# Performance work log

Hardware: AMD Instinct MI355X
Metric: run time of the kernel (lower is better)

## Reference

```python
import jax, jax.numpy as jnp
import numpy as np

D_MODEL, N_HEADS, D_K, D_V = 1024, 16, 64, 64
B, S = 4, 2048
EPS = 1e-5


def setup_inputs() -> dict:
    key = jax.random.key(0)
    ks = jax.random.split(key, 8)
    scale = 1.0 / np.sqrt(D_MODEL)
    return {
        "input_Q": jax.random.normal(ks[0], (B, S, D_MODEL), dtype=jnp.float32),
        "input_K": jax.random.normal(ks[1], (B, S, D_MODEL), dtype=jnp.float32),
        "input_V": jax.random.normal(ks[2], (B, S, D_MODEL), dtype=jnp.float32),
        "attn_mask": jax.random.bernoulli(ks[3], 0.15, (B, S, S)),  # True = masked
        "W_Q": jax.random.uniform(ks[4], (N_HEADS * D_K, D_MODEL), jnp.float32, -scale, scale),
        "W_K": jax.random.uniform(ks[5], (N_HEADS * D_K, D_MODEL), jnp.float32, -scale, scale),
        "W_V": jax.random.uniform(ks[6], (N_HEADS * D_V, D_MODEL), jnp.float32, -scale, scale),
        "W_fc": jax.random.uniform(ks[7], (D_MODEL, N_HEADS * D_V), jnp.float32, -scale, scale),
    }


def _proj(x, W, h, d):
    # x: [B,S,D] @ W.T ([D, h*d]) -> [B,h,S,d]
    b, s, _ = x.shape
    y = jnp.einsum("bsd,ed->bse", x, W)
    return y.reshape(b, s, h, d).transpose(0, 2, 1, 3)


def reference(input_Q, input_K, input_V, attn_mask, W_Q, W_K, W_V, W_fc):
    b, s, d_model = input_Q.shape
    Q = _proj(input_Q, W_Q, N_HEADS, D_K)  # [B,H,S,dk]
    K = _proj(input_K, W_K, N_HEADS, D_K)
    V = _proj(input_V, W_V, N_HEADS, D_V)

    scores = jnp.einsum("bhqd,bhkd->bhqk", Q, K) / np.sqrt(D_K).astype(np.float32)
    scores = jnp.where(attn_mask[:, None, :, :], jnp.float32(-1e9), scores)
    attn = jax.nn.softmax(scores, axis=-1)  # [B,H,S,S]

    context = jnp.einsum("bhqk,bhkd->bhqd", attn, V)
    context = context.transpose(0, 2, 1, 3).reshape(b, s, N_HEADS * D_V)
    output = jnp.einsum("bse,de->bsd", context, W_fc)

    x = output + input_Q  # residual
    mu = jnp.mean(x, axis=-1, keepdims=True)
    var = jnp.mean(jnp.square(x - mu), axis=-1, keepdims=True)
    ln = (x - mu) / jnp.sqrt(var + EPS)  # fresh LayerNorm: gamma=1, beta=0
    return ln, attn
```

## Files before the change

### kernel.cpp

```cpp
#include <hip/hip_runtime.h>
#include <cstdint>
#include <cstddef>

constexpr int Bc  = 4;
constexpr int Sc  = 2048;
constexpr int DMc = 1024;
constexpr int Hc  = 16;
constexpr int DHc = 64;
constexpr int BHc = Bc * Hc;

typedef float f32x4  __attribute__((ext_vector_type(4)));
typedef short bf16x8 __attribute__((ext_vector_type(8)));

static __device__ __forceinline__ short f2bf(float x) {
  uint32_t u = __builtin_bit_cast(uint32_t, x);
  u += 0x7fffu + ((u >> 16) & 1u);
  return (short)(u >> 16);
}

static __device__ __forceinline__ f32x4 mfma16(bf16x8 a, bf16x8 b, f32x4 c) {
  return __builtin_amdgcn_mfma_f32_16x16x32_bf16(a, b, c, 0, 0, 0);
}

static __device__ __forceinline__ void gload16(const short* g, short* l) {
  __builtin_amdgcn_global_load_lds(
      (const __attribute__((address_space(1))) void*)g,
      (__attribute__((address_space(3))) void*)l, 16, 0, 0);
}

__global__ __launch_bounds__(256) void k_cvt(const float* __restrict__ in,
                                             short* __restrict__ out) {
  int i = blockIdx.x * 256 + threadIdx.x;
  float4 v = reinterpret_cast<const float4*>(in)[i];
  short4 o;
  o.x = f2bf(v.x); o.y = f2bf(v.y); o.z = f2bf(v.z); o.w = f2bf(v.w);
  reinterpret_cast<short4*>(out)[i] = o;
}

__global__ __launch_bounds__(256) void k_pack(const int* __restrict__ m,
                                              uint32_t* __restrict__ bits) {
  size_t i = (size_t)blockIdx.x * 256 + threadIdx.x;
  uint64_t b = __ballot(m[i] != 0);
  int lane = threadIdx.x & 63;
  if (lane == 0)  bits[i >> 5] = (uint32_t)b;
  if (lane == 32) bits[i >> 5] = (uint32_t)(b >> 32);
}

__global__ __launch_bounds__(256) void k_gemm(const short* __restrict__ A,
                                              const short* __restrict__ Bt,
                                              void* __restrict__ out, int mode) {
  __shared__ __align__(16) short lA[128 * 32];
  __shared__ __align__(16) short lB[128 * 32];
  const int bm = blockIdx.x * 128, bn = blockIdx.y * 128;
  const int lane = threadIdx.x & 63, w = threadIdx.x >> 6;
  const int wr = w >> 1, wc = w & 1;
  const int r = lane & 15, g = lane >> 4;
  const int lrow = lane >> 2;
  const int lsl  = (lane & 3) ^ ((lane >> 3) & 3);
  const int rsw  = (r >> 1) & 3;

  f32x4 acc[4][4] = {};
  const short* Ab = A + (size_t)bm * DMc;
  const short* Bb = Bt + (size_t)bn * DMc;

  for (int k0 = 0; k0 < DMc; k0 += 32) {
    __syncthreads();
    #pragma unroll
    for (int c = 0; c < 2; c++) {
      const int rbase = c * 64 + w * 16;
      gload16(Ab + (size_t)(rbase + lrow) * DMc + k0 + lsl * 8, lA + rbase * 32);
      gload16(Bb + (size_t)(rbase + lrow) * DMc + k0 + lsl * 8, lB + rbase * 32);
    }
    __syncthreads();

    bf16x8 af[4], bfr[4];
    #pragma unroll
    for (int i = 0; i < 4; i++) {
      const int arow = wr * 64 + i * 16 + r;
      af[i]  = *reinterpret_cast<const bf16x8*>(lA + arow * 32 + (g ^ rsw) * 8);
      const int brow = wc * 64 + i * 16 + r;
      bfr[i] = *reinterpret_cast<const bf16x8*>(lB + brow * 32 + (g ^ rsw) * 8);
    }
    #pragma unroll
    for (int i = 0; i < 4; i++)
      #pragma unroll
      for (int n = 0; n < 4; n++) acc[i][n] = mfma16(af[i], bfr[n], acc[i][n]);
  }

  #pragma unroll
  for (int i = 0; i < 4; i++) {
    #pragma unroll
    for (int n = 0; n < 4; n++) {
      const int col = bn + wc * 64 + n * 16 + r;
      #pragma unroll
      for (int j = 0; j < 4; j++) {
        const int m = bm + wr * 64 + i * 16 + g * 4 + j;
        if (mode == 2) {
          reinterpret_cast<float*>(out)[(size_t)m * DMc + col] = acc[i][n][j];
        } else {
          const int b = m >> 11, s = m & (Sc - 1);
          const int h = col >> 6, d = col & (DHc - 1);
          size_t idx = (mode == 1)
              ? ((size_t)(b * Hc + h) * DHc + d) * Sc + s
              : ((size_t)(b * Hc + h) * Sc + s) * DHc + d;
          reinterpret_cast<short*>(out)[idx] = f2bf(acc[i][n][j]);
        }
      }
    }
  }
}

__global__ __launch_bounds__(512, 4) void k_flash(const short* __restrict__ Qb,
                                                  const short* __restrict__ Kb,
                                                  const short* __restrict__ Vt,
                                                  const uint32_t* __restrict__ pbits,
                                                  short* __restrict__ ctx,
                                                  float* __restrict__ rsum) {
  __shared__ __align__(16) short kbuf[2][4096];
  __shared__ __align__(16) short vbuf[2][4096];
  __shared__ __align__(16) short pbuf[8][1024];

  const int qbase = blockIdx.x * 128;
  const int bh = blockIdx.y;
  const int b = bh >> 4, h = bh & 15;
  const int tid = threadIdx.x;
  const int lane = tid & 63, w = tid >> 6;
  const int r = lane & 15, g = lane >> 4;
  const int rx = r & 7;

  const int srow = tid >> 3;
  const int sslot = (tid & 7) ^ (srow & 7);
  const short* ksrc = Kb + ((size_t)bh * Sc + srow) * DHc + sslot * 8;
  const short* vsrc = Vt + ((size_t)bh * DHc + srow) * Sc + sslot * 8;
  short* const kdst0 = &kbuf[0][w * 512];
  short* const kdst1 = &kbuf[1][w * 512];
  short* const vdst0 = &vbuf[0][w * 512];
  short* const vdst1 = &vbuf[1][w * 512];

  const short* qrow = Qb + ((size_t)bh * Sc + qbase + w * 16 + r) * DHc;
  const bf16x8 qf0 = *reinterpret_cast<const bf16x8*>(qrow + g * 8);
  const bf16x8 qf1 = *reinterpret_cast<const bf16x8*>(qrow + g * 8 + 32);

  const uint32_t* mrow = pbits + ((size_t)b * Sc + qbase + w * 16 + r) * (Sc / 32);

  constexpr float SCL = 0.18033688f;
  f32x4 pacc[4] = {};
  float rs = 0.f;

  gload16(ksrc, kdst0);
  gload16(vsrc, vdst0);
  __syncthreads();

  int cur = 0;
  for (int kt = 0; kt < 32; kt++) {
    if (kt + 1 < 32) {
      gload16(ksrc + (size_t)(kt + 1) * 64 * DHc, cur ? kdst0 : kdst1);
      gload16(vsrc + (kt + 1) * 64,               cur ? vdst0 : vdst1);
    }
    const short* kb = kbuf[cur];
    const short* vb = vbuf[cur];

    f32x4 sc4[4];
    #pragma unroll
    for (int tt = 0; tt < 4; tt++) {
      const int krow = (tt * 16 + r) * 64;
      bf16x8 kf0 = *reinterpret_cast<const bf16x8*>(kb + krow + ((g ^ rx) << 3));
      bf16x8 kf1 = *reinterpret_cast<const bf16x8*>(kb + krow + (((g + 4) ^ rx) << 3));
      f32x4 a = {};
      a = mfma16(kf0, qf0, a);
      a = mfma16(kf1, qf1, a);
      sc4[tt] = a;
    }

    const uint2 mu = *reinterpret_cast<const uint2*>(mrow + kt * 2);
    #pragma unroll
    for (int tt = 0; tt < 4; tt++) {
      const uint32_t mword = (tt < 2) ? mu.x : mu.y;
      const int bsh = (tt & 1) * 16 + g * 4;
      f32x4 e;
      #pragma unroll
      for (int j = 0; j < 4; j++) {
        float v = __builtin_exp2f(sc4[tt][j] * SCL);
        if ((mword >> (bsh + j)) & 1u) v = 0.f;
        e[j] = v;
        rs += v;
      }
      uint32_t lo = (uint32_t)(uint16_t)f2bf(e[0]) | ((uint32_t)(uint16_t)f2bf(e[1]) << 16);
      uint32_t hi = (uint32_t)(uint16_t)f2bf(e[2]) | ((uint32_t)(uint16_t)f2bf(e[3]) << 16);
      uint64_t pk = (uint64_t)lo | ((uint64_t)hi << 32);
      *reinterpret_cast<uint64_t*>(
          &pbuf[w][r * 64 + (((tt * 2 + (g >> 1)) ^ rx) << 3) + ((g & 1) << 2)]) = pk;
    }

    #pragma unroll
    for (int kt2 = 0; kt2 < 2; kt2++) {
      const int sl = ((kt2 * 4 + g) ^ rx) << 3;
      const bf16x8 paf = *reinterpret_cast<const bf16x8*>(&pbuf[w][r * 64 + sl]);
      #pragma unroll
      for (int n = 0; n < 4; n++) {
        const bf16x8 vf = *reinterpret_cast<const bf16x8*>(vb + (n * 16 + r) * 64 + sl);
        pacc[n] = mfma16(paf, vf, pacc[n]);
      }
    }

    __syncthreads();
    cur ^= 1;
  }

  rs += __shfl_xor(rs, 16);
  rs += __shfl_xor(rs, 32);

  float riv[4];
  #pragma unroll
  for (int j = 0; j < 4; j++) riv[j] = 1.0f / __shfl(rs, g * 4 + j);

  short* cbase = ctx + ((size_t)b * Sc + qbase + w * 16) * DMc + h * DHc;
  #pragma unroll
  for (int n = 0; n < 4; n++)
    #pragma unroll
    for (int j = 0; j < 4; j++)
      cbase[(size_t)(g * 4 + j) * DMc + n * 16 + r] = f2bf(pacc[n][j] * riv[j]);

  if (lane < 16) rsum[(size_t)bh * Sc + qbase + w * 16 + r] = rs;
}

__global__ __launch_bounds__(512) void k_attnw(const short* __restrict__ Qb,
                                               const short* __restrict__ Kb,
                                               const uint32_t* __restrict__ pbits,
                                               const float* __restrict__ rsum,
                                               float* __restrict__ attn) {
  const int qb = blockIdx.x * 16;
  const int bh = blockIdx.y;
  const int b = bh >> 4;
  const int lane = threadIdx.x & 63, w = threadIdx.x >> 6;
  const int r = lane & 15, g = lane >> 4;

  const short* qrow = Qb + ((size_t)bh * Sc + qb + r) * DHc;
  const bf16x8 qf0 = *reinterpret_cast<const bf16x8*>(qrow + g * 8);
  const bf16x8 qf1 = *reinterpret_cast<const bf16x8*>(qrow + g * 8 + 32);

  const float rinv = 1.0f / rsum[(size_t)bh * Sc + qb + r];

  const uint32_t* mrow = pbits + ((size_t)b * Sc + qb + r) * (Sc / 32) + w * 8;
  const uint4 m0 = *reinterpret_cast<const uint4*>(mrow);
  const uint4 m1 = *reinterpret_cast<const uint4*>(mrow + 4);
  const uint32_t mw[8] = {m0.x, m0.y, m0.z, m0.w, m1.x, m1.y, m1.z, m1.w};

  const short* kbase = Kb + ((size_t)bh * Sc + w * 256) * DHc;
  float* out = attn + ((size_t)bh * Sc + qb + r) * Sc + w * 256;

  constexpr float SCL = 0.18033688f;
  #pragma unroll
  for (int t = 0; t < 16; t++) {
    const short* krow = kbase + (size_t)(t * 16 + r) * DHc;
    bf16x8 kf0 = *reinterpret_cast<const bf16x8*>(krow + g * 8);
    bf16x8 kf1 = *reinterpret_cast<const bf16x8*>(krow + g * 8 + 32);
    f32x4 a = {};
    a = mfma16(kf0, qf0, a);
    a = mfma16(kf1, qf1, a);
    const uint32_t mword = mw[t >> 1];
    const int bsh = (t & 1) * 16 + g * 4;
    f32x4 o;
    #pragma unroll
    for (int j = 0; j < 4; j++) {
      float v = __builtin_exp2f(a[j] * SCL) * rinv;
      if ((mword >> (bsh + j)) & 1u) v = 0.f;
      o[j] = v;
    }
    __builtin_nontemporal_store(o, reinterpret_cast<f32x4*>(out + t * 16 + g * 4));
  }
}

__global__ __launch_bounds__(256) void k_ln(const float* __restrict__ y,
                                            const float* __restrict__ resid,
                                            float* __restrict__ out) {
  const int m = blockIdx.x, t = threadIdx.x;
  const float4 a = reinterpret_cast<const float4*>(y + (size_t)m * DMc)[t];
  const float4 b = reinterpret_cast<const float4*>(resid + (size_t)m * DMc)[t];
  float x0 = a.x + b.x, x1 = a.y + b.y, x2 = a.z + b.z, x3 = a.w + b.w;

  float s = x0 + x1 + x2 + x3;
  #pragma unroll
  for (int m2 = 1; m2 < 64; m2 <<= 1) s += __shfl_xor(s, m2);
  __shared__ float red[4];
  __shared__ float red2[4];
  const int w = t >> 6, lane = t & 63;
  if (lane == 0) red[w] = s;
  __syncthreads();
  const float mean = (red[0] + red[1] + red[2] + red[3]) * (1.0f / DMc);

  x0 -= mean; x1 -= mean; x2 -= mean; x3 -= mean;
  float s2 = x0 * x0 + x1 * x1 + x2 * x2 + x3 * x3;
  #pragma unroll
  for (int m2 = 1; m2 < 64; m2 <<= 1) s2 += __shfl_xor(s2, m2);
  if (lane == 0) red2[w] = s2;
  __syncthreads();
  const float var = (red2[0] + red2[1] + red2[2] + red2[3]) * (1.0f / DMc);
  const float rstd = rsqrtf(var + 1e-5f);

  float4 o;
  o.x = x0 * rstd; o.y = x1 * rstd; o.z = x2 * rstd; o.w = x3 * rstd;
  reinterpret_cast<float4*>(out + (size_t)m * DMc)[t] = o;
}

extern "C" void kernel_launch(void* const* d_in, const int* in_sizes, int n_in,
                              void* d_out, int out_size, void* d_ws, size_t ws_size,
                              hipStream_t stream) {
  const float* inQ = (const float*)d_in[0];
  const float* inK = (const float*)d_in[1];
  const float* inV = (const float*)d_in[2];
  const int*   msk = (const int*)d_in[3];
  const float* WQ  = (const float*)d_in[4];
  const float* WK  = (const float*)d_in[5];
  const float* WV  = (const float*)d_in[6];
  const float* Wfc = (const float*)d_in[7];

  float* out_ln   = (float*)d_out;
  float* out_attn = out_ln + (size_t)Bc * Sc * DMc;

  const size_t NX = (size_t)Bc * Sc * DMc;
  const size_t NW = (size_t)DMc * DMc;
  short* ws = (short*)d_ws;
  short* XbQ = ws;
  short* XbK = XbQ + NX;
  short* XbV = XbK + NX;
  short* WQb = XbV + NX;
  short* WKb = WQb + NW;
  short* WVb = WKb + NW;
  short* Wfb = WVb + NW;
  short* Qb  = Wfb + NW;
  short* Kb  = Qb + NX;
  short* Vt  = Kb + NX;
  uint32_t* pbits = (uint32_t*)(Vt + NX);
  float* rsum = (float*)(pbits + (size_t)Bc * Sc * (Sc / 32));
  short* ctx = XbV;
  float* y   = (float*)XbQ;

  k_cvt<<<dim3((unsigned)(NX / 1024)), 256, 0, stream>>>(inQ, XbQ);
  k_cvt<<<dim3((unsigned)(NX / 1024)), 256, 0, stream>>>(inK, XbK);
  k_cvt<<<dim3((unsigned)(NX / 1024)), 256, 0, stream>>>(inV, XbV);
  k_cvt<<<dim3((unsigned)(NW / 1024)), 256, 0, stream>>>(WQ, WQb);
  k_cvt<<<dim3((unsigned)(NW / 1024)), 256, 0, stream>>>(WK, WKb);
  k_cvt<<<dim3((unsigned)(NW / 1024)), 256, 0, stream>>>(WV, WVb);
  k_cvt<<<dim3((unsigned)(NW / 1024)), 256, 0, stream>>>(Wfc, Wfb);
  k_pack<<<dim3((unsigned)(Bc * Sc * (Sc / 256))), 256, 0, stream>>>(msk, pbits);

  dim3 gp(Bc * Sc / 128, DMc / 128);
  k_gemm<<<gp, 256, 0, stream>>>(XbQ, WQb, (void*)Qb, 0);
  k_gemm<<<gp, 256, 0, stream>>>(XbK, WKb, (void*)Kb, 0);
  k_gemm<<<gp, 256, 0, stream>>>(XbV, WVb, (void*)Vt, 1);

  k_flash<<<dim3(Sc / 128, BHc), 512, 0, stream>>>(Qb, Kb, Vt, pbits, ctx, rsum);

  k_attnw<<<dim3(Sc / 16, BHc), 512, 0, stream>>>(Qb, Kb, pbits, rsum, out_attn);

  k_gemm<<<gp, 256, 0, stream>>>(ctx, Wfb, (void*)y, 2);

  k_ln<<<dim3(Bc * Sc), 256, 0, stream>>>(y, inQ, out_ln);
}
```

Before: 654.0 us.

## Fuse attention-weight output into flash kernel and batch conversion/QKV GEMM launches

Moves the second pass that writes the normalized attention matrix into the end of the flash kernel, using the row sum already held in registers, so the separate attnw kernel and the rsum buffer go away. The seven conversion launches are merged into two kernels, and the three QKV projection GEMMs into one launch using a z grid dimension with templated modes. This cuts launch overhead and the rsum round trip. The cost is a flash kernel whose tail is now dominated by streaming 1 GB of attention writes from only 128-row blocks, which may lower the parallelism available for that write phase.

After: 597.2 us. 1.1x faster.

```diff
diff --git a/kernel.cpp b/kernel.cpp
--- a/kernel.cpp
+++ b/kernel.cpp
@@ -28,8 +28,32 @@
       (__attribute__((address_space(3))) void*)l, 16, 0, 0);
 }
 
-__global__ __launch_bounds__(256) void k_cvt(const float* __restrict__ in,
-                                             short* __restrict__ out) {
+__global__ __launch_bounds__(256) void k_cvt3(const float* __restrict__ a,
+                                              const float* __restrict__ b,
+                                              const float* __restrict__ c,
+                                              short* __restrict__ oa,
+                                              short* __restrict__ ob,
+                                              short* __restrict__ oc) {
+  const float* in = blockIdx.y == 0 ? a : (blockIdx.y == 1 ? b : c);
+  short* out      = blockIdx.y == 0 ? oa : (blockIdx.y == 1 ? ob : oc);
+  int i = blockIdx.x * 256 + threadIdx.x;
+  float4 v = reinterpret_cast<const float4*>(in)[i];
+  short4 o;
+  o.x = f2bf(v.x); o.y = f2bf(v.y); o.z = f2bf(v.z); o.w = f2bf(v.w);
+  reinterpret_cast<short4*>(out)[i] = o;
+}
+
+__global__ __launch_bounds__(256) void k_cvtw(const float* __restrict__ a,
+                                              const float* __restrict__ b,
+                                              const float* __restrict__ c,
+                                              const float* __restrict__ d,
+                                              short* __restrict__ oa,
+                                              short* __restrict__ ob,
+                                              short* __restrict__ oc,
+                                              short* __restrict__ od) {
+  const int y = blockIdx.y;
+  const float* in = y == 0 ? a : (y == 1 ? b : (y == 2 ? c : d));
+  short* out      = y == 0 ? oa : (y == 1 ? ob : (y == 2 ? oc : od));
   int i = blockIdx.x * 256 + threadIdx.x;
   float4 v = reinterpret_cast<const float4*>(in)[i];
   short4 o;
@@ -46,12 +70,13 @@
   if (lane == 32) bits[i >> 5] = (uint32_t)(b >> 32);
 }
 
-__global__ __launch_bounds__(256) void k_gemm(const short* __restrict__ A,
-                                              const short* __restrict__ Bt,
-                                              void* __restrict__ out, int mode) {
+template <int MODE>
+static __device__ __forceinline__ void gemm_body(const short* __restrict__ A,
+                                                 const short* __restrict__ Bt,
+                                                 void* __restrict__ out,
+                                                 int bm, int bn) {
   __shared__ __align__(16) short lA[128 * 32];
   __shared__ __align__(16) short lB[128 * 32];
-  const int bm = blockIdx.x * 128, bn = blockIdx.y * 128;
   const int lane = threadIdx.x & 63, w = threadIdx.x >> 6;
   const int wr = w >> 1, wc = w & 1;
   const int r = lane & 15, g = lane >> 4;
@@ -95,12 +120,12 @@
       #pragma unroll
       for (int j = 0; j < 4; j++) {
         const int m = bm + wr * 64 + i * 16 + g * 4 + j;
-        if (mode == 2) {
+        if (MODE == 2) {
           reinterpret_cast<float*>(out)[(size_t)m * DMc + col] = acc[i][n][j];
         } else {
           const int b = m >> 11, s = m & (Sc - 1);
           const int h = col >> 6, d = col & (DHc - 1);
-          size_t idx = (mode == 1)
+          size_t idx = (MODE == 1)
               ? ((size_t)(b * Hc + h) * DHc + d) * Sc + s
               : ((size_t)(b * Hc + h) * Sc + s) * DHc + d;
           reinterpret_cast<short*>(out)[idx] = f2bf(acc[i][n][j]);
@@ -110,12 +135,34 @@
   }
 }
 
-__global__ __launch_bounds__(512, 4) void k_flash(const short* __restrict__ Qb,
-                                                  const short* __restrict__ Kb,
-                                                  const short* __restrict__ Vt,
-                                                  const uint32_t* __restrict__ pbits,
-                                                  short* __restrict__ ctx,
-                                                  float* __restrict__ rsum) {
+__global__ __launch_bounds__(256) void k_gemmQKV(const short* __restrict__ XQ,
+                                                 const short* __restrict__ XK,
+                                                 const short* __restrict__ XV,
+                                                 const short* __restrict__ WQ,
+                                                 const short* __restrict__ WK,
+                                                 const short* __restrict__ WV,
+                                                 short* __restrict__ Q,
+                                                 short* __restrict__ K,
+                                                 short* __restrict__ V) {
+  const int z = blockIdx.z;
+  const int bm = blockIdx.x * 128, bn = blockIdx.y * 128;
+  if (z == 0)      gemm_body<0>(XQ, WQ, (void*)Q, bm, bn);
+  else if (z == 1) gemm_body<0>(XK, WK, (void*)K, bm, bn);
+  else             gemm_body<1>(XV, WV, (void*)V, bm, bn);
+}
+
+__global__ __launch_bounds__(256) void k_gemmO(const short* __restrict__ A,
+                                               const short* __restrict__ Bt,
+                                               float* __restrict__ out) {
+  gemm_body<2>(A, Bt, (void*)out, blockIdx.x * 128, blockIdx.y * 128);
+}
+
+__global__ __launch_bounds__(512, 4) void k_flash2(const short* __restrict__ Qb,
+                                                   const short* __restrict__ Kb,
+                                                   const short* __restrict__ Vt,
+                                                   const uint32_t* __restrict__ pbits,
+                                                   short* __restrict__ ctx,
+                                                   float* __restrict__ attn) {
   __shared__ __align__(16) short kbuf[2][4096];
   __shared__ __align__(16) short vbuf[2][4096];
   __shared__ __align__(16) short pbuf[8][1024];
@@ -209,6 +256,7 @@
 
   rs += __shfl_xor(rs, 16);
   rs += __shfl_xor(rs, 32);
+  const float rinv = 1.0f / rs;
 
   float riv[4];
   #pragma unroll
@@ -221,53 +269,31 @@
     for (int j = 0; j < 4; j++)
       cbase[(size_t)(g * 4 + j) * DMc + n * 16 + r] = f2bf(pacc[n][j] * riv[j]);
 
-  if (lane < 16) rsum[(size_t)bh * Sc + qbase + w * 16 + r] = rs;
-}
-
-__global__ __launch_bounds__(512) void k_attnw(const short* __restrict__ Qb,
-                                               const short* __restrict__ Kb,
-                                               const uint32_t* __restrict__ pbits,
-                                               const float* __restrict__ rsum,
-                                               float* __restrict__ attn) {
-  const int qb = blockIdx.x * 16;
-  const int bh = blockIdx.y;
-  const int b = bh >> 4;
-  const int lane = threadIdx.x & 63, w = threadIdx.x >> 6;
-  const int r = lane & 15, g = lane >> 4;
-
-  const short* qrow = Qb + ((size_t)bh * Sc + qb + r) * DHc;
-  const bf16x8 qf0 = *reinterpret_cast<const bf16x8*>(qrow + g * 8);
-  const bf16x8 qf1 = *reinterpret_cast<const bf16x8*>(qrow + g * 8 + 32);
-
-  const float rinv = 1.0f / rsum[(size_t)bh * Sc + qb + r];
-
-  const uint32_t* mrow = pbits + ((size_t)b * Sc + qb + r) * (Sc / 32) + w * 8;
-  const uint4 m0 = *reinterpret_cast<const uint4*>(mrow);
-  const uint4 m1 = *reinterpret_cast<const uint4*>(mrow + 4);
-  const uint32_t mw[8] = {m0.x, m0.y, m0.z, m0.w, m1.x, m1.y, m1.z, m1.w};
-
-  const short* kbase = Kb + ((size_t)bh * Sc + w * 256) * DHc;
-  float* out = attn + ((size_t)bh * Sc + qb + r) * Sc + w * 256;
-
-  constexpr float SCL = 0.18033688f;
-  #pragma unroll
-  for (int t = 0; t < 16; t++) {
-    const short* krow = kbase + (size_t)(t * 16 + r) * DHc;
-    bf16x8 kf0 = *reinterpret_cast<const bf16x8*>(krow + g * 8);
-    bf16x8 kf1 = *reinterpret_cast<const bf16x8*>(krow + g * 8 + 32);
-    f32x4 a = {};
-    a = mfma16(kf0, qf0, a);
-    a = mfma16(kf1, qf1, a);
-    const uint32_t mword = mw[t >> 1];
-    const int bsh = (t & 1) * 16 + g * 4;
-    f32x4 o;
-    #pragma unroll
-    for (int j = 0; j < 4; j++) {
-      float v = __builtin_exp2f(a[j] * SCL) * rinv;
-      if ((mword >> (bsh + j)) & 1u) v = 0.f;
-      o[j] = v;
-    }
-    __builtin_nontemporal_store(o, reinterpret_cast<f32x4*>(out + t * 16 + g * 4));
+  const short* kbase = Kb + (size_t)bh * Sc * DHc;
+  float* out = attn + ((size_t)bh * Sc + qbase + w * 16 + r) * Sc;
+  #pragma unroll 2
+  for (int kt = 0; kt < 32; kt++) {
+    const uint2 mu = *reinterpret_cast<const uint2*>(mrow + kt * 2);
+    #pragma unroll
+    for (int tt = 0; tt < 4; tt++) {
+      const short* krow = kbase + (size_t)(kt * 64 + tt * 16 + r) * DHc;
+      bf16x8 kf0 = *reinterpret_cast<const bf16x8*>(krow + g * 8);
+      bf16x8 kf1 = *reinterpret_cast<const bf16x8*>(krow + g * 8 + 32);
+      f32x4 a = {};
+      a = mfma16(kf0, qf0, a);
+      a = mfma16(kf1, qf1, a);
+      const uint32_t mword = (tt < 2) ? mu.x : mu.y;
+      const int bsh = (tt & 1) * 16 + g * 4;
+      f32x4 o;
+      #pragma unroll
+      for (int j = 0; j < 4; j++) {
+        float v = __builtin_exp2f(a[j] * SCL) * rinv;
+        if ((mword >> (bsh + j)) & 1u) v = 0.f;
+        o[j] = v;
+      }
+      __builtin_nontemporal_store(
+          o, reinterpret_cast<f32x4*>(out + kt * 64 + tt * 16 + g * 4));
+    }
   }
 }
 
@@ -332,29 +358,20 @@
   short* Kb  = Qb + NX;
   short* Vt  = Kb + NX;
   uint32_t* pbits = (uint32_t*)(Vt + NX);
-  float* rsum = (float*)(pbits + (size_t)Bc * Sc * (Sc / 32));
   short* ctx = XbV;
   float* y   = (float*)XbQ;
 
-  k_cvt<<<dim3((unsigned)(NX / 1024)), 256, 0, stream>>>(inQ, XbQ);
-  k_cvt<<<dim3((unsigned)(NX / 1024)), 256, 0, stream>>>(inK, XbK);
-  k_cvt<<<dim3((unsigned)(NX / 1024)), 256, 0, stream>>>(inV, XbV);
-  k_cvt<<<dim3((unsigned)(NW / 1024)), 256, 0, stream>>>(WQ, WQb);
-  k_cvt<<<dim3((unsigned)(NW / 1024)), 256, 0, stream>>>(WK, WKb);
-  k_cvt<<<dim3((unsigned)(NW / 1024)), 256, 0, stream>>>(WV, WVb);
-  k_cvt<<<dim3((unsigned)(NW / 1024)), 256, 0, stream>>>(Wfc, Wfb);
+  k_cvt3<<<dim3((unsigned)(NX / 1024), 3), 256, 0, stream>>>(inQ, inK, inV, XbQ, XbK, XbV);
+  k_cvtw<<<dim3((unsigned)(NW / 1024), 4), 256, 0, stream>>>(WQ, WK, WV, Wfc,
+                                                             WQb, WKb, WVb, Wfb);
   k_pack<<<dim3((unsigned)(Bc * Sc * (Sc / 256))), 256, 0, stream>>>(msk, pbits);
 
-  dim3 gp(Bc * Sc / 128, DMc / 128);
-  k_gemm<<<gp, 256, 0, stream>>>(XbQ, WQb, (void*)Qb, 0);
-  k_gemm<<<gp, 256, 0, stream>>>(XbK, WKb, (void*)Kb, 0);
-  k_gemm<<<gp, 256, 0, stream>>>(XbV, WVb, (void*)Vt, 1);
-
-  k_flash<<<dim3(Sc / 128, BHc), 512, 0, stream>>>(Qb, Kb, Vt, pbits, ctx, rsum);
-
-  k_attnw<<<dim3(Sc / 16, BHc), 512, 0, stream>>>(Qb, Kb, pbits, rsum, out_attn);
-
-  k_gemm<<<gp, 256, 0, stream>>>(ctx, Wfb, (void*)y, 2);
+  k_gemmQKV<<<dim3(Bc * Sc / 128, DMc / 128, 3), 256, 0, stream>>>(
+      XbQ, XbK, XbV, WQb, WKb, WVb, Qb, Kb, Vt);
+
+  k_flash2<<<dim3(Sc / 128, BHc), 512, 0, stream>>>(Qb, Kb, Vt, pbits, ctx, out_attn);
+
+  k_gemmO<<<dim3(Bc * Sc / 128, DMc / 128), 256, 0, stream>>>(ctx, Wfb, y);
 
   k_ln<<<dim3(Bc * Sc), 256, 0, stream>>>(y, inQ, out_ln);
 }
```
